# Optimization experiments

Measured on AMD Instinct MI355X. Metric: run time of the kernel, lower is better.

## Reference

```python
import jax, jax.numpy as jnp
import numpy as np

# DeformConv3d hyperparams (from init_kwargs)
STRIDE = (1, 1, 1)
PAD = (1, 1, 1)
DIL = (1, 1, 1)
GROUPS = 1
DEFORM_GROUPS = 1  # reference assumes dg == 1


def setup_inputs() -> dict:
    key = jax.random.key(0)
    k1, k2, k3, k4 = jax.random.split(key, 4)
    x = jax.random.normal(k1, (2, 32, 24, 24, 24), jnp.float32)
    # offset channels = 3 * dg * kD*kH*kW = 81, layout [k_idx, (dz,dy,dx)]
    offset = jax.random.normal(k2, (2, 81, 24, 24, 24), jnp.float32)
    weight = jax.random.normal(k3, (64, 32, 3, 3, 3), jnp.float32) * 0.05
    bias = jax.random.normal(k4, (64,), jnp.float32) * 0.05
    return {"x": x, "offset": offset, "weight": weight, "bias": bias}


def _deform_conv3d(x, offset, weight, bias):
    B, C, D, H, W = x.shape
    Cout, Cg, kD, kH, kW = weight.shape
    sD, sH, sW = STRIDE
    pD, pH, pW = PAD
    dD, dH, dW = DIL
    Kn = kD * kH * kW
    Do = (D + 2 * pD - dD * (kD - 1) - 1) // sD + 1
    Ho = (H + 2 * pH - dH * (kH - 1) - 1) // sH + 1
    Wo = (W + 2 * pW - dW * (kW - 1) - 1) // sW + 1
    N = Do * Ho * Wo

    # offset: [B, Kn*3, Do,Ho,Wo] -> [B, Kn, 3, N]
    off = offset.reshape(B, Kn, 3, N)

    # kernel tap grid [Kn]
    kz, ky, kx = jnp.meshgrid(jnp.arange(kD), jnp.arange(kH), jnp.arange(kW), indexing='ij')
    kz, ky, kx = kz.reshape(Kn), ky.reshape(Kn), kx.reshape(Kn)
    # output grid [N]
    oz, oy, ox = jnp.meshgrid(jnp.arange(Do), jnp.arange(Ho), jnp.arange(Wo), indexing='ij')
    oz, oy, ox = oz.reshape(N), oy.reshape(N), ox.reshape(N)

    # sampling coords [B, Kn, N]
    z = (oz[None, None, :] * sD - pD) + kz[None, :, None] * dD + off[:, :, 0]
    y = (oy[None, None, :] * sH - pH) + ky[None, :, None] * dH + off[:, :, 1]
    xx = (ox[None, None, :] * sW - pW) + kx[None, :, None] * dW + off[:, :, 2]

    z0 = jnp.floor(z); fz = z - z0
    y0 = jnp.floor(y); fy = y - y0
    x0 = jnp.floor(xx); fx = xx - x0

    x_flat = x.reshape(B, C, D * H * W)
    acc = jnp.zeros((B, C, Kn * N), x.dtype)
    # 8 trilinear corners (fixed small loop)
    for dz in (0, 1):
        iz = z0 + dz
        wz = fz if dz else (1.0 - fz)
        for dy in (0, 1):
            iy = y0 + dy
            wy = fy if dy else (1.0 - fy)
            for dx in (0, 1):
                ix = x0 + dx
                wx = fx if dx else (1.0 - fx)
                valid = ((iz >= 0) & (iz < D) & (iy >= 0) & (iy < H)
                         & (ix >= 0) & (ix < W))
                w = (wz * wy * wx) * valid.astype(x.dtype)  # [B,Kn,N]
                izc = jnp.clip(iz, 0, D - 1).astype(jnp.int32)
                iyc = jnp.clip(iy, 0, H - 1).astype(jnp.int32)
                ixc = jnp.clip(ix, 0, W - 1).astype(jnp.int32)
                idx = (izc * H + iyc) * W + ixc  # [B,Kn,N]
                g = jnp.take_along_axis(x_flat, idx.reshape(B, 1, Kn * N), axis=2)
                acc = acc + g * w.reshape(B, 1, Kn * N)

    # im2col columns ordered (c, kz, ky, kx) to match weight layout
    cols = acc.reshape(B, C * Kn, N)
    Cpg = C // GROUPS
    Opg = Cout // GROUPS
    cols_g = cols.reshape(B, GROUPS, Cpg * Kn, N)
    w_g = weight.reshape(GROUPS, Opg, Cpg * Kn)
    out = jnp.einsum('gok,bgkn->bgon', w_g, cols_g).reshape(B, Cout, N)
    out = out + bias[None, :, None]
    return out.reshape(B, Cout, Do, Ho, Wo)


def reference(x, offset, weight, bias):
    return _deform_conv3d(x, offset, weight, bias)
```

## Files before the change

kernel.cpp:

```cpp
#include <hip/hip_runtime.h>
#include <hip/hip_fp16.h>


constexpr int B   = 2;
constexpr int C   = 32;
constexpr int D   = 24, H = 24, W = 24;
constexpr int CO  = 64;
constexpr int KN  = 27;
constexpr int DHW = D * H * W;
constexpr int N   = DHW;
constexpr int CK  = C * KN;

constexpr int NPOS     = 16;
constexpr int NTAP     = NPOS * KN;
constexpr int TPB_MAIN = 448;
constexpr int PADR     = CK + 8;
constexpr int NBLK     = (B * N) / NPOS;

constexpr int PREPX_BLKS = (B * DHW * 4) / 256;
constexpr int PREPW_BLKS = (CO * CK) / 256;

using h8v   = __attribute__((ext_vector_type(8))) _Float16;
using f32x4 = __attribute__((ext_vector_type(4))) float;

__device__ __forceinline__ h8v splat8(float w) {
    const _Float16 h = (_Float16)w;
    h8v r;
    #pragma unroll
    for (int i = 0; i < 8; ++i) r[i] = h;
    return r;
}

__global__ __launch_bounds__(256)
void prep_fused(const float* __restrict__ x, const float* __restrict__ wgt,
                _Float16* __restrict__ xT, _Float16* __restrict__ wp) {
    const int bid = blockIdx.x;
    if (bid < PREPX_BLKS) {
        const int idx = bid * 256 + threadIdx.x;
        const int v   = idx >> 2;
        const int q   = idx & 3;
        const int b   = v / DHW;
        const int vox = v - b * DHW;
        const float* src = x + ((size_t)(b * C + q * 8)) * DHW + vox;
        _Float16 tmp[8];
        #pragma unroll
        for (int i = 0; i < 8; ++i) tmp[i] = (_Float16)src[(size_t)i * DHW];
        *reinterpret_cast<int4*>(xT + (size_t)v * 32 + q * 8) =
            *reinterpret_cast<const int4*>(tmp);
    } else {
        const int idx   = (bid - PREPX_BLKS) * 256 + threadIdx.x;
        const int j     = idx & 7;
        const int lane  = (idx >> 3) & 63;
        const int t     = idx >> 9;
        const int otile = t / 27;
        const int kstep = t - otile * 27;
        const int o     = otile * 16 + (lane & 15);
        const int c     = 8 * (lane >> 4) + j;
        wp[idx] = (_Float16)wgt[(size_t)o * CK + c * KN + kstep];
    }
}

__global__ __launch_bounds__(TPB_MAIN)
void deform_main(const float* __restrict__ off,
                 const _Float16* __restrict__ xT,
                 const _Float16* __restrict__ wp,
                 const float* __restrict__ bias,
                 float* __restrict__ out) {
    __shared__ _Float16 s_vb[NPOS * PADR];

    const int tid   = threadIdx.x;
    const int blk   = blockIdx.x;
    const int n0    = blk * NPOS;
    const int b     = n0 / N;
    const int nbase = n0 - b * N;

    if (tid < NTAP) {
        const int p = tid & 15;
        const int k = tid >> 4;
        const int n = nbase + p;
        const int oz = n / 576;
        const int rr = n - oz * 576;
        const int oy = rr / 24;
        const int ox = rr - oy * 24;
        const int kz = k / 9;
        const int kr = k - kz * 9;
        const int ky = kr / 3;
        const int kx = kr - ky * 3;

        const float offz = off[((size_t)(b * 81 + k * 3 + 0)) * N + n];
        const float offy = off[((size_t)(b * 81 + k * 3 + 1)) * N + n];
        const float offx = off[((size_t)(b * 81 + k * 3 + 2)) * N + n];

        const float z  = (float)(oz - 1 + kz) + offz;
        const float y  = (float)(oy - 1 + ky) + offy;
        const float xx = (float)(ox - 1 + kx) + offx;
        const float zf = floorf(z), yf = floorf(y), xf = floorf(xx);
        const float fz = z - zf, fy = y - yf, fx = xx - xf;
        const int z0 = (int)zf, y0 = (int)yf, x0 = (int)xf;

        int   cidx[8];
        float cw[8];
        #pragma unroll
        for (int cr = 0; cr < 8; ++cr) {
            const int cz = cr >> 2, cy = (cr >> 1) & 1, cx = cr & 1;
            const int iz = z0 + cz, iy = y0 + cy, ix = x0 + cx;
            const bool vd = ((unsigned)iz < (unsigned)D) &&
                            ((unsigned)iy < (unsigned)H) &&
                            ((unsigned)ix < (unsigned)W);
            const int izc = min(max(iz, 0), D - 1);
            const int iyc = min(max(iy, 0), H - 1);
            const int ixc = min(max(ix, 0), W - 1);
            cidx[cr] = (izc * H + iyc) * W + ixc;
            const float wz = cz ? fz : 1.0f - fz;
            const float wy = cy ? fy : 1.0f - fy;
            const float wx = cx ? fx : 1.0f - fx;
            cw[cr] = vd ? (wz * wy * wx) : 0.0f;
        }

        h8v acc0 = splat8(0.0f), acc1 = splat8(0.0f),
            acc2 = splat8(0.0f), acc3 = splat8(0.0f);
        const h8v* base = reinterpret_cast<const h8v*>(xT) + (size_t)b * DHW * 4;

        #pragma unroll
        for (int hb = 0; hb < 2; ++hb) {
            h8v v[4][4];
            #pragma unroll
            for (int cr = 0; cr < 4; ++cr) {
                const h8v* s = base + (size_t)cidx[hb * 4 + cr] * 4;
                v[cr][0] = s[0]; v[cr][1] = s[1];
                v[cr][2] = s[2]; v[cr][3] = s[3];
            }
            #pragma unroll
            for (int cr = 0; cr < 4; ++cr) {
                const h8v w8 = splat8(cw[hb * 4 + cr]);
                acc0 += v[cr][0] * w8;
                acc1 += v[cr][1] * w8;
                acc2 += v[cr][2] * w8;
                acc3 += v[cr][3] * w8;
            }
        }

        h8v* dst = reinterpret_cast<h8v*>(&s_vb[p * PADR + k * 32]);
        dst[0] = acc0; dst[1] = acc1; dst[2] = acc2; dst[3] = acc3;
    }
    __syncthreads();

    const int wv = tid >> 6;
    if (wv < 4) {
        const int lane = tid & 63;
        f32x4 acc4 = {0.f, 0.f, 0.f, 0.f};
        const h8v* wrow = reinterpret_cast<const h8v*>(wp) + (wv * 27) * 64 + lane;
        const int lrow = (lane & 15) * PADR;
        const int lcol = (lane >> 4) * 8;
        #pragma unroll
        for (int ks = 0; ks < 27; ++ks) {
            const h8v a  = wrow[ks * 64];
            const h8v bf = *reinterpret_cast<const h8v*>(&s_vb[lrow + ks * 32 + lcol]);
            acc4 = __builtin_amdgcn_mfma_f32_16x16x32_f16(a, bf, acc4, 0, 0, 0);
        }
        const int p = lane & 15;
        const int n = nbase + p;
        const int obase = wv * 16 + (lane >> 4) * 4;
        #pragma unroll
        for (int r = 0; r < 4; ++r) {
            const int o = obase + r;
            out[((size_t)(b * CO + o)) * N + n] = acc4[r] + bias[o];
        }
    }
}

extern "C" void kernel_launch(void* const* d_in, const int* in_sizes, int n_in,
                              void* d_out, int out_size, void* d_ws, size_t ws_size,
                              hipStream_t stream) {
    const float* x    = (const float*)d_in[0];
    const float* off  = (const float*)d_in[1];
    const float* wgt  = (const float*)d_in[2];
    const float* bias = (const float*)d_in[3];
    float* out = (float*)d_out;

    _Float16* xT = (_Float16*)d_ws;
    _Float16* wp = (_Float16*)((char*)d_ws + 1769472);

    prep_fused<<<PREPX_BLKS + PREPW_BLKS, 256, 0, stream>>>(x, wgt, xT, wp);
    deform_main<<<NBLK, TPB_MAIN, 0, stream>>>(off, xT, wp, bias, out);
}
```

Baseline: 109.9 us.

## Split gather across channel quarters, double positions per block, transpose x via LDS

```diff
diff --git a/kernel.cpp b/kernel.cpp
--- a/kernel.cpp
+++ b/kernel.cpp
@@ -11,13 +11,14 @@
 constexpr int N   = DHW;
 constexpr int CK  = C * KN;
 
-constexpr int NPOS     = 16;
+constexpr int NPOS     = 32;
 constexpr int NTAP     = NPOS * KN;
-constexpr int TPB_MAIN = 448;
+constexpr int NTASK    = NTAP * 4;
+constexpr int TPB_MAIN = 576;
 constexpr int PADR     = CK + 8;
 constexpr int NBLK     = (B * N) / NPOS;
 
-constexpr int PREPX_BLKS = (B * DHW * 4) / 256;
+constexpr int PREPX_BLKS = (B * DHW) / 256;
 constexpr int PREPW_BLKS = (CO * CK) / 256;
 
 using h8v   = __attribute__((ext_vector_type(8))) _Float16;
@@ -31,22 +32,40 @@
     return r;
 }
 
+__device__ __forceinline__ unsigned pack2h(float a, float b) {
+    const _Float16 ha = (_Float16)a, hb = (_Float16)b;
+    unsigned short ua, ub;
+    __builtin_memcpy(&ua, &ha, 2);
+    __builtin_memcpy(&ub, &hb, 2);
+    return (unsigned)ua | ((unsigned)ub << 16);
+}
+
 __global__ __launch_bounds__(256)
 void prep_fused(const float* __restrict__ x, const float* __restrict__ wgt,
                 _Float16* __restrict__ xT, _Float16* __restrict__ wp) {
     const int bid = blockIdx.x;
     if (bid < PREPX_BLKS) {
-        const int idx = bid * 256 + threadIdx.x;
-        const int v   = idx >> 2;
-        const int q   = idx & 3;
-        const int b   = v / DHW;
-        const int vox = v - b * DHW;
-        const float* src = x + ((size_t)(b * C + q * 8)) * DHW + vox;
-        _Float16 tmp[8];
+        __shared__ unsigned s_t[256 * 21];
+        const int tid = threadIdx.x;
+        const int v0  = bid * 256;
+        const int b   = (v0 >= DHW) ? 1 : 0;
+        const int vox = (v0 - b * DHW) + tid;
+        const float* xb = x + (size_t)(b * C) * DHW + vox;
         #pragma unroll
-        for (int i = 0; i < 8; ++i) tmp[i] = (_Float16)src[(size_t)i * DHW];
-        *reinterpret_cast<int4*>(xT + (size_t)v * 32 + q * 8) =
-            *reinterpret_cast<const int4*>(tmp);
+        for (int c2 = 0; c2 < 16; ++c2) {
+            const float f0 = xb[(size_t)(2 * c2)     * DHW];
+            const float f1 = xb[(size_t)(2 * c2 + 1) * DHW];
+            s_t[tid * 21 + c2] = pack2h(f0, f1);
+        }
+        __syncthreads();
+        unsigned r[16];
+        #pragma unroll
+        for (int j = 0; j < 16; ++j) r[j] = s_t[tid * 21 + j];
+        int4* dst = reinterpret_cast<int4*>(xT + ((size_t)(v0 + tid)) * 32);
+        dst[0] = make_int4(r[0],  r[1],  r[2],  r[3]);
+        dst[1] = make_int4(r[4],  r[5],  r[6],  r[7]);
+        dst[2] = make_int4(r[8],  r[9],  r[10], r[11]);
+        dst[3] = make_int4(r[12], r[13], r[14], r[15]);
     } else {
         const int idx   = (bid - PREPX_BLKS) * 256 + threadIdx.x;
         const int j     = idx & 7;
@@ -60,7 +79,7 @@
     }
 }
 
-__global__ __launch_bounds__(TPB_MAIN)
+__global__ __launch_bounds__(TPB_MAIN, 5)
 void deform_main(const float* __restrict__ off,
                  const _Float16* __restrict__ xT,
                  const _Float16* __restrict__ wp,
@@ -73,11 +92,17 @@
     const int n0    = blk * NPOS;
     const int b     = n0 / N;
     const int nbase = n0 - b * N;
+    const h8v* xbase = reinterpret_cast<const h8v*>(xT) + (size_t)b * DHW * 4;
+    const float* offb = off + (size_t)(b * 81) * N;
 
-    if (tid < NTAP) {
-        const int p = tid & 15;
-        const int k = tid >> 4;
-        const int n = nbase + p;
+    #pragma unroll 1
+    for (int r = 0; r < 6; ++r) {
+        const int tau = tid + r * TPB_MAIN;
+        const int q   = tau & 3;
+        const int tap = tau >> 2;
+        const int p   = tap & 31;
+        const int k   = tap >> 5;
+        const int n   = nbase + p;
         const int oz = n / 576;
         const int rr = n - oz * 576;
         const int oy = rr / 24;
@@ -87,9 +112,9 @@
         const int ky = kr / 3;
         const int kx = kr - ky * 3;
 
-        const float offz = off[((size_t)(b * 81 + k * 3 + 0)) * N + n];
-        const float offy = off[((size_t)(b * 81 + k * 3 + 1)) * N + n];
-        const float offx = off[((size_t)(b * 81 + k * 3 + 2)) * N + n];
+        const float offz = offb[((size_t)(k * 3 + 0)) * N + n];
+        const float offy = offb[((size_t)(k * 3 + 1)) * N + n];
+        const float offx = offb[((size_t)(k * 3 + 2)) * N + n];
 
         const float z  = (float)(oz - 1 + kz) + offz;
         const float y  = (float)(oy - 1 + ky) + offy;
@@ -117,40 +142,28 @@
             cw[cr] = vd ? (wz * wy * wx) : 0.0f;
         }
 
-        h8v acc0 = splat8(0.0f), acc1 = splat8(0.0f),
-            acc2 = splat8(0.0f), acc3 = splat8(0.0f);
-        const h8v* base = reinterpret_cast<const h8v*>(xT) + (size_t)b * DHW * 4;
+        h8v v[8];
+        #pragma unroll
+        for (int cr = 0; cr < 8; ++cr)
+            v[cr] = xbase[(size_t)cidx[cr] * 4 + q];
+        h8v acc = splat8(0.0f);
+        #pragma unroll
+        for (int cr = 0; cr < 8; ++cr)
+            acc += v[cr] * splat8(cw[cr]);
 
-        #pragma unroll
-        for (int hb = 0; hb < 2; ++hb) {
-            h8v v[4][4];
-            #pragma unroll
-            for (int cr = 0; cr < 4; ++cr) {
-                const h8v* s = base + (size_t)cidx[hb * 4 + cr] * 4;
-                v[cr][0] = s[0]; v[cr][1] = s[1];
-                v[cr][2] = s[2]; v[cr][3] = s[3];
-            }
-            #pragma unroll
-            for (int cr = 0; cr < 4; ++cr) {
-                const h8v w8 = splat8(cw[hb * 4 + cr]);
-                acc0 += v[cr][0] * w8;
-                acc1 += v[cr][1] * w8;
-                acc2 += v[cr][2] * w8;
-                acc3 += v[cr][3] * w8;
-            }
-        }
-
-        h8v* dst = reinterpret_cast<h8v*>(&s_vb[p * PADR + k * 32]);
-        dst[0] = acc0; dst[1] = acc1; dst[2] = acc2; dst[3] = acc3;
+        *reinterpret_cast<h8v*>(&s_vb[p * PADR + k * 32 + q * 8]) = acc;
     }
     __syncthreads();
 
     const int wv = tid >> 6;
-    if (wv < 4) {
+    if (wv < 8) {
         const int lane = tid & 63;
+        const int ot   = wv & 3;
+        const int pt   = wv >> 2;
+        const int p    = pt * 16 + (lane & 15);
         f32x4 acc4 = {0.f, 0.f, 0.f, 0.f};
-        const h8v* wrow = reinterpret_cast<const h8v*>(wp) + (wv * 27) * 64 + lane;
-        const int lrow = (lane & 15) * PADR;
+        const h8v* wrow = reinterpret_cast<const h8v*>(wp) + (ot * 27) * 64 + lane;
+        const int lrow = p * PADR;
         const int lcol = (lane >> 4) * 8;
         #pragma unroll
         for (int ks = 0; ks < 27; ++ks) {
@@ -158,13 +171,12 @@
             const h8v bf = *reinterpret_cast<const h8v*>(&s_vb[lrow + ks * 32 + lcol]);
             acc4 = __builtin_amdgcn_mfma_f32_16x16x32_f16(a, bf, acc4, 0, 0, 0);
         }
-        const int p = lane & 15;
         const int n = nbase + p;
-        const int obase = wv * 16 + (lane >> 4) * 4;
+        const int obase = ot * 16 + (lane >> 4) * 4;
         #pragma unroll
-        for (int r = 0; r < 4; ++r) {
-            const int o = obase + r;
-            out[((size_t)(b * CO + o)) * N + n] = acc4[r] + bias[o];
+        for (int rr = 0; rr < 4; ++rr) {
+            const int o = obase + rr;
+            out[((size_t)(b * CO + o)) * N + n] = acc4[rr] + bias[o];
         }
     }
 }
```

Measured after the change: 100.1 us. 1.1x faster.
